# Kernel optimization log

Measured on AMD Instinct MI355X. Metric: run time of the kernel, lower is better.

## Reference

```python
import jax, jax.numpy as jnp
import numpy as np

OUT_DIM = 4096
NCROPS = 10
STUDENT_TEMP = 0.1
WARMUP_TEACHER_TEMP = 0.04
TEACHER_TEMP = 0.07
WARMUP_EPOCHS = 30
NEPOCHS = 100
B = 32
NG = 196
NL = 36
DFEAT = 384


def _l2norm(x, eps=1e-12):
    n = jnp.sqrt(jnp.sum(x * x, axis=-1, keepdims=True))
    return x / jnp.maximum(n, eps)


def setup_inputs() -> dict:
    key = jax.random.key(0)
    ks = jax.random.split(key, 6)
    s_rows = B * (2 * NG + (NCROPS - 2) * NL)  # 21760
    t_rows = 2 * B * NG  # 12544
    return {
        "student_cls_pred": jax.random.normal(ks[0], (NCROPS * B, OUT_DIM), jnp.float32),
        "student_region_pred": jax.random.normal(ks[1], (s_rows, OUT_DIM), jnp.float32),
        "student_feats": jax.random.normal(ks[2], (s_rows, DFEAT), jnp.float32),
        "teacher_cls_pred": jax.random.normal(ks[3], (2 * B, OUT_DIM), jnp.float32),
        "teacher_region_pred": jax.random.normal(ks[4], (t_rows, OUT_DIM), jnp.float32),
        "teacher_feats": jax.random.normal(ks[5], (t_rows, DFEAT), jnp.float32),
        "center": jnp.zeros((1, OUT_DIM), jnp.float32),
        "center_grid": jnp.zeros((1, OUT_DIM), jnp.float32),
        "epoch": 50,
        "n_global": 196,
        "n_local": 36,
    }


def reference(student_cls_pred, student_region_pred, student_feats,
              teacher_cls_pred, teacher_region_pred, teacher_feats,
              center, center_grid, epoch, n_global, n_local):
    sched = np.concatenate((np.linspace(WARMUP_TEACHER_TEMP, TEACHER_TEMP, WARMUP_EPOCHS),
                            np.ones(NEPOCHS - WARMUP_EPOCHS) * TEACHER_TEMP))
    temp = float(sched[epoch])

    b = teacher_cls_pred.shape[0] // 2
    N = n_global

    # teacher targets (detached in torch)
    t_cls = jax.lax.stop_gradient(jax.nn.softmax((teacher_cls_pred - center) / temp, axis=-1))
    t_reg = jax.lax.stop_gradient(jax.nn.softmax((teacher_region_pred - center_grid) / temp, axis=-1))
    t_cls_chunks = jnp.split(t_cls, 2, axis=0)
    t_reg_chunks = jnp.split(t_reg, 2, axis=0)
    t_fea_chunks = jnp.split(teacher_feats, 2, axis=0)

    s_cls = student_cls_pred / STUDENT_TEMP
    s_cls_chunks = jnp.split(s_cls, NCROPS, axis=0)

    split_sizes = [n_global] * 2 + [n_local] * (NCROPS - 2)
    offsets = np.cumsum([0] + [s * b for s in split_sizes])
    s_reg_scaled = student_region_pred / STUDENT_TEMP
    s_reg_chunks = [s_reg_scaled[offsets[k]:offsets[k + 1]] for k in range(NCROPS)]
    s_fea_chunks = [student_feats[offsets[k]:offsets[k + 1]] for k in range(NCROPS)]

    total_loss = jnp.zeros((), student_cls_pred.dtype)
    n_terms = 0
    for i in range(2):
        q = t_cls_chunks[i]                                   # [b, D]
        t_region = t_reg_chunks[i].reshape(b, N, -1)          # [b, N, D]
        t_fea = _l2norm(t_fea_chunks[i].reshape(b, N, -1))    # [b, N, F]
        for j in range(NCROPS):
            if j == i:
                continue
            v = s_cls_chunks[j]
            loss = 0.5 * jnp.sum(-q * jax.nn.log_softmax(v, axis=-1), axis=-1)  # [b]

            S = split_sizes[j]
            s_region = s_reg_chunks[j].reshape(b, S, -1)      # [b, S, D]
            s_fea = _l2norm(s_fea_chunks[j].reshape(b, S, -1))
            sim = jnp.einsum('bsf,bnf->bsn', s_fea, t_fea)    # cosine sim [b, S, N]
            ind = jnp.argmax(sim, axis=2)                     # [b, S]
            t_indexed = jnp.take_along_axis(t_region, ind[:, :, None], axis=1)  # [b, S, D]
            loss = loss + 0.5 * jnp.mean(
                jnp.sum(-t_indexed * jax.nn.log_softmax(s_region, axis=-1), axis=-1), axis=-1)
            total_loss = total_loss + jnp.mean(loss)
            n_terms += 1
    return total_loss / n_terms
```

## Files before the change

kernel.cpp:

```cpp
#include <hip/hip_runtime.h>
#include <math.h>

#define D 4096
#define F 384
#define NB 32
#define NG 196
#define NL 36
#define SROWS 21760
#define TROWS 12544
#define TCHUNK 6272
#define LCHUNK 1152
#define NPART (SROWS + 576)
#define KT 32
#define PADW 68

__device__ inline float get_invtemp(const int* ep_ptr) {
  int ep = *ep_ptr;
  double t = (ep < 30) ? (0.04 + (double)ep * (0.03 / 29.0)) : 0.07;
  return 1.0f / (float)t;
}

__device__ inline float warp_max(float v) {
#pragma unroll
  for (int o = 32; o; o >>= 1) v = fmaxf(v, __shfl_xor(v, o));
  return v;
}
__device__ inline float warp_sum(float v) {
#pragma unroll
  for (int o = 32; o; o >>= 1) v += __shfl_xor(v, o);
  return v;
}
__device__ inline float block_max(float v, float* sc) {
  v = warp_max(v);
  __syncthreads();
  if ((threadIdx.x & 63) == 0) sc[threadIdx.x >> 6] = v;
  __syncthreads();
  return fmaxf(fmaxf(sc[0], sc[1]), fmaxf(sc[2], sc[3]));
}
__device__ inline float block_sum(float v, float* sc) {
  v = warp_sum(v);
  __syncthreads();
  if ((threadIdx.x & 63) == 0) sc[threadIdx.x >> 6] = v;
  __syncthreads();
  return (sc[0] + sc[1]) + (sc[2] + sc[3]);
}

__device__ inline unsigned long long umax64(unsigned long long a, unsigned long long b) {
  return a > b ? a : b;
}
__device__ inline unsigned long long pack_key(float sim, int tc) {
  unsigned bts = __float_as_uint(sim);
  bts = (bts & 0x80000000u) ? ~bts : (bts | 0x80000000u);
  return ((unsigned long long)bts << 32) | (unsigned long long)(0xFFFFFFFFu - (unsigned)tc);
}
__device__ inline void unpack4(float4 v, float* dst) {
  dst[0] = v.x; dst[1] = v.y; dst[2] = v.z; dst[3] = v.w;
}

__device__ inline int srow_of(int cat, int b, int p) {
  if (cat == 0) return b * NG + p;
  if (cat == 1) return TCHUNK + b * NG + p;
  int j = p / 36;
  int pos = p - j * 36;
  return 2 * TCHUNK + j * LCHUNK + b * NL + pos;
}

__global__ __launch_bounds__(256) void k_tnorm(const float* __restrict__ tfea,
                                               float* __restrict__ invtn) {
  int gw = (blockIdx.x * 256 + threadIdx.x) >> 6;
  int lane = threadIdx.x & 63;
  if (gw >= TROWS) return;
  const float* p = tfea + (size_t)gw * F;
  float ss = 0.f;
#pragma unroll
  for (int k = 0; k < 6; k++) { float v = p[lane + 64 * k]; ss += v * v; }
  ss = warp_sum(ss);
  if (lane == 0) invtn[gw] = 1.0f / fmaxf(sqrtf(ss), 1e-12f);
}

__global__ __launch_bounds__(256) void k_sim(const float* __restrict__ sfea,
                                             const float* __restrict__ tfea,
                                             const float* __restrict__ invtn,
                                             unsigned long long* __restrict__ keys) {
  __shared__ float s_km[KT][PADW];
  __shared__ float tA_km[KT][PADW];
  __shared__ float tB_km[KT][PADW];
  int tid = threadIdx.x;
  int bid = blockIdx.x;
  int tt = bid & 3;
  int rest = bid >> 2;
  int st = rest % 13;
  int b = rest / 13;
  int cat, base_p;
  if (st < 4)      { cat = 0; base_p = st * 64; }
  else if (st < 8) { cat = 1; base_p = (st - 4) * 64; }
  else             { cat = 2; base_p = (st - 8) * 64; }
  int vs = ((cat < 2) ? NG : 288) - base_p; if (vs > 64) vs = 64;
  bool ni2 = (cat == 2);
  int iA = (cat == 0) ? 1 : 0;
  int tc0 = tt * 64;
  int vt = NG - tc0; if (vt > 64) vt = 64;
  int gA = iA * TCHUNK + b * NG + tc0;
  int gB = TCHUNK + b * NG + tc0;
  int tx = tid & 15, ty = tid >> 4;

  int row0 = tid >> 3, c4 = tid & 7;
  int row1 = row0 + 32;
  bool sv0 = row0 < vs, sv1 = row1 < vs;
  bool tv0 = row0 < vt, tv1 = row1 < vt;
  const float* sp0 = sfea + (size_t)srow_of(cat, b, base_p + (sv0 ? row0 : 0)) * F + c4 * 4;
  const float* sp1 = sfea + (size_t)srow_of(cat, b, base_p + (sv1 ? row1 : 0)) * F + c4 * 4;
  const float* tpA0 = tfea + (size_t)(gA + (tv0 ? row0 : 0)) * F + c4 * 4;
  const float* tpA1 = tfea + (size_t)(gA + (tv1 ? row1 : 0)) * F + c4 * 4;
  const float* tpB0 = tfea + (size_t)(gB + (tv0 ? row0 : 0)) * F + c4 * 4;
  const float* tpB1 = tfea + (size_t)(gB + (tv1 ? row1 : 0)) * F + c4 * 4;
  int kbase = c4 * 4;

  float accA[4][4] = {{0.f}}, accB[4][4] = {{0.f}};
  const float4 z4 = make_float4(0.f, 0.f, 0.f, 0.f);

  for (int kt = 0; kt < F / KT; kt++) {
    int k0 = kt * KT;
    float4 a0 = sv0 ? *(const float4*)(sp0 + k0) : z4;
    float4 a1 = sv1 ? *(const float4*)(sp1 + k0) : z4;
    float4 b0 = tv0 ? *(const float4*)(tpA0 + k0) : z4;
    float4 b1 = tv1 ? *(const float4*)(tpA1 + k0) : z4;
    float4 c0 = z4, c1 = z4;
    if (ni2) {
      c0 = tv0 ? *(const float4*)(tpB0 + k0) : z4;
      c1 = tv1 ? *(const float4*)(tpB1 + k0) : z4;
    }
    __syncthreads();
    s_km[kbase + 0][row0] = a0.x; s_km[kbase + 1][row0] = a0.y;
    s_km[kbase + 2][row0] = a0.z; s_km[kbase + 3][row0] = a0.w;
    s_km[kbase + 0][row1] = a1.x; s_km[kbase + 1][row1] = a1.y;
    s_km[kbase + 2][row1] = a1.z; s_km[kbase + 3][row1] = a1.w;
    tA_km[kbase + 0][row0] = b0.x; tA_km[kbase + 1][row0] = b0.y;
    tA_km[kbase + 2][row0] = b0.z; tA_km[kbase + 3][row0] = b0.w;
    tA_km[kbase + 0][row1] = b1.x; tA_km[kbase + 1][row1] = b1.y;
    tA_km[kbase + 2][row1] = b1.z; tA_km[kbase + 3][row1] = b1.w;
    if (ni2) {
      tB_km[kbase + 0][row0] = c0.x; tB_km[kbase + 1][row0] = c0.y;
      tB_km[kbase + 2][row0] = c0.z; tB_km[kbase + 3][row0] = c0.w;
      tB_km[kbase + 0][row1] = c1.x; tB_km[kbase + 1][row1] = c1.y;
      tB_km[kbase + 2][row1] = c1.z; tB_km[kbase + 3][row1] = c1.w;
    }
    __syncthreads();
    if (ni2) {
#pragma unroll 8
      for (int kk = 0; kk < KT; kk++) {
        float4 s4 = *(const float4*)&s_km[kk][ty * 4];
        float4 t4 = *(const float4*)&tA_km[kk][tx * 4];
        float4 u4 = *(const float4*)&tB_km[kk][tx * 4];
        float sv[4], tv[4], uv[4];
        unpack4(s4, sv); unpack4(t4, tv); unpack4(u4, uv);
#pragma unroll
        for (int m = 0; m < 4; m++)
#pragma unroll
          for (int n = 0; n < 4; n++) {
            accA[m][n] += sv[m] * tv[n];
            accB[m][n] += sv[m] * uv[n];
          }
      }
    } else {
#pragma unroll 8
      for (int kk = 0; kk < KT; kk++) {
        float4 s4 = *(const float4*)&s_km[kk][ty * 4];
        float4 t4 = *(const float4*)&tA_km[kk][tx * 4];
        float sv[4], tv[4];
        unpack4(s4, sv); unpack4(t4, tv);
#pragma unroll
        for (int m = 0; m < 4; m++)
#pragma unroll
          for (int n = 0; n < 4; n++) accA[m][n] += sv[m] * tv[n];
      }
    }
  }

  float invA[4], invB[4];
#pragma unroll
  for (int n = 0; n < 4; n++) {
    int tcl = tx * 4 + n;
    invA[n] = (tcl < vt) ? invtn[gA + tcl] : 0.f;
    invB[n] = (ni2 && tcl < vt) ? invtn[gB + tcl] : 0.f;
  }
#pragma unroll
  for (int m = 0; m < 4; m++) {
    int sl = ty * 4 + m;
    unsigned long long bestA = 0ull, bestB = 0ull;
#pragma unroll
    for (int n = 0; n < 4; n++) {
      int tcl = tx * 4 + n;
      if (tcl < vt) {
        int tc = tc0 + tcl;
        bestA = umax64(bestA, pack_key(accA[m][n] * invA[n], tc));
        if (ni2) bestB = umax64(bestB, pack_key(accB[m][n] * invB[n], tc));
      }
    }
#pragma unroll
    for (int o = 1; o < 16; o <<= 1) {
      bestA = umax64(bestA, __shfl_xor(bestA, o));
      bestB = umax64(bestB, __shfl_xor(bestB, o));
    }
    if (tx == 0 && sl < vs) {
      int sr = srow_of(cat, b, base_p + sl);
      atomicMax(&keys[(size_t)iA * SROWS + sr], bestA);
      if (ni2) atomicMax(&keys[(size_t)SROWS + sr], bestB);
    }
  }
}

__global__ __launch_bounds__(256) void k_region(const float* __restrict__ sreg,
                                                const float* __restrict__ treg,
                                                const float* __restrict__ cgrid,
                                                const unsigned long long* __restrict__ keys,
                                                const int* __restrict__ epoch,
                                                float* __restrict__ partials) {
  __shared__ float sc[4];
  int r = blockIdx.x, tid = threadIdx.x;
  int j, rem;
  if (r < TCHUNK)          { j = 0; rem = r; }
  else if (r < 2 * TCHUNK) { j = 1; rem = r - TCHUNK; }
  else { int q = r - 2 * TCHUNK; j = 2 + q / LCHUNK; rem = q - (j - 2) * LCHUNK; }
  int S = (j < 2) ? NG : NL;
  int b = rem / S;
  float invtemp = get_invtemp(epoch);

  const float4* sp = (const float4*)(sreg + (size_t)r * D);
  float sv[16];
  unpack4(sp[tid], sv); unpack4(sp[tid + 256], sv + 4);
  unpack4(sp[tid + 512], sv + 8); unpack4(sp[tid + 768], sv + 12);
#pragma unroll
  for (int k = 0; k < 16; k++) sv[k] *= 10.f;

  float m = -INFINITY;
#pragma unroll
  for (int k = 0; k < 16; k++) m = fmaxf(m, sv[k]);
  float M = block_max(m, sc);
  float e = 0.f;
#pragma unroll
  for (int k = 0; k < 16; k++) e += expf(sv[k] - M);
  float Ssum = block_sum(e, sc);
  float base = M + logf(Ssum);

  const float4* cp = (const float4*)cgrid;
  float cv[16];
  unpack4(cp[tid], cv); unpack4(cp[tid + 256], cv + 4);
  unpack4(cp[tid + 512], cv + 8); unpack4(cp[tid + 768], cv + 12);

  int ni = (j >= 2) ? 2 : 1;
  int i0 = (j == 0) ? 1 : 0;
  float wsel = 0.5f / (float)(S * NB * 18);
  float acc = 0.f;
  for (int q = 0; q < ni; q++) {
    int i = (q == 0) ? i0 : 1;
    unsigned long long kv = keys[(size_t)i * SROWS + r];
    int ind = (int)(0xFFFFFFFFu - (unsigned)(kv & 0xFFFFFFFFull));
    const float4* tp = (const float4*)(treg + (size_t)(i * TCHUNK + b * NG + ind) * D);
    float tv[16];
    unpack4(tp[tid], tv); unpack4(tp[tid + 256], tv + 4);
    unpack4(tp[tid + 512], tv + 8); unpack4(tp[tid + 768], tv + 12);
#pragma unroll
    for (int k = 0; k < 16; k++) tv[k] = (tv[k] - cv[k]) * invtemp;
    float tm = -INFINITY;
#pragma unroll
    for (int k = 0; k < 16; k++) tm = fmaxf(tm, tv[k]);
    float Tm = block_max(tm, sc);
    float es = 0.f, ed = 0.f;
#pragma unroll
    for (int k = 0; k < 16; k++) {
      float ee = expf(tv[k] - Tm);
      es += ee; ed += ee * sv[k];
    }
    es = block_sum(es, sc);
    ed = block_sum(ed, sc);
    acc += wsel * (base - ed / es);
  }
  if (tid == 0) partials[r] = acc;
}

__global__ __launch_bounds__(256) void k_cls(const float* __restrict__ scls,
                                             const float* __restrict__ tcls,
                                             const float* __restrict__ center,
                                             const int* __restrict__ epoch,
                                             float* __restrict__ part) {
  __shared__ float sc[4];
  int bid = blockIdx.x, tid = threadIdx.x;
  int p = bid >> 5, b = bid & 31;
  int i = p / 9, jj = p % 9;
  int j = (jj < i) ? jj : jj + 1;
  float invtemp = get_invtemp(epoch);

  const float4* sp = (const float4*)(scls + (size_t)(j * NB + b) * D);
  float sv[16];
  unpack4(sp[tid], sv); unpack4(sp[tid + 256], sv + 4);
  unpack4(sp[tid + 512], sv + 8); unpack4(sp[tid + 768], sv + 12);
#pragma unroll
  for (int k = 0; k < 16; k++) sv[k] *= 10.f;
  float m = -INFINITY;
#pragma unroll
  for (int k = 0; k < 16; k++) m = fmaxf(m, sv[k]);
  float M = block_max(m, sc);
  float e = 0.f;
#pragma unroll
  for (int k = 0; k < 16; k++) e += expf(sv[k] - M);
  float Ssum = block_sum(e, sc);
  float base = M + logf(Ssum);

  const float4* cp = (const float4*)center;
  const float4* tp = (const float4*)(tcls + (size_t)(i * NB + b) * D);
  float tv[16], cv[16];
  unpack4(cp[tid], cv); unpack4(cp[tid + 256], cv + 4);
  unpack4(cp[tid + 512], cv + 8); unpack4(cp[tid + 768], cv + 12);
  unpack4(tp[tid], tv); unpack4(tp[tid + 256], tv + 4);
  unpack4(tp[tid + 512], tv + 8); unpack4(tp[tid + 768], tv + 12);
#pragma unroll
  for (int k = 0; k < 16; k++) tv[k] = (tv[k] - cv[k]) * invtemp;
  float tm = -INFINITY;
#pragma unroll
  for (int k = 0; k < 16; k++) tm = fmaxf(tm, tv[k]);
  float Tm = block_max(tm, sc);
  float es = 0.f, ed = 0.f;
#pragma unroll
  for (int k = 0; k < 16; k++) {
    float ee = expf(tv[k] - Tm);
    es += ee; ed += ee * sv[k];
  }
  es = block_sum(es, sc);
  ed = block_sum(ed, sc);
  if (tid == 0) part[bid] = (base - ed / es) * (0.5f / 576.f);
}

__global__ __launch_bounds__(1024) void k_final(const float* __restrict__ partials,
                                                float* __restrict__ out, int n) {
  __shared__ float sc[16];
  int tid = threadIdx.x;
  float s = 0.f;
  for (int idx = tid; idx < n; idx += 1024) s += partials[idx];
  s = warp_sum(s);
  if ((tid & 63) == 0) sc[tid >> 6] = s;
  __syncthreads();
  if (tid < 64) {
    float v = (tid < 16) ? sc[tid] : 0.f;
    v = warp_sum(v);
    if (tid == 0) out[0] = v;
  }
}

extern "C" void kernel_launch(void* const* d_in, const int* in_sizes, int n_in,
                              void* d_out, int out_size, void* d_ws, size_t ws_size,
                              hipStream_t stream) {
  const float* s_cls = (const float*)d_in[0];
  const float* s_reg = (const float*)d_in[1];
  const float* s_fea = (const float*)d_in[2];
  const float* t_cls = (const float*)d_in[3];
  const float* t_reg = (const float*)d_in[4];
  const float* t_fea = (const float*)d_in[5];
  const float* center = (const float*)d_in[6];
  const float* cgrid = (const float*)d_in[7];
  const int* epoch = (const int*)d_in[8];

  char* ws = (char*)d_ws;
  unsigned long long* keys = (unsigned long long*)ws;
  float* invtn = (float*)(ws + 348160);
  float* partials = (float*)(ws + 398336);

  hipMemsetAsync(keys, 0, (size_t)2 * SROWS * sizeof(unsigned long long), stream);
  k_tnorm<<<TROWS / 4, 256, 0, stream>>>(t_fea, invtn);
  k_sim<<<32 * 13 * 4, 256, 0, stream>>>(s_fea, t_fea, invtn, keys);
  k_region<<<SROWS, 256, 0, stream>>>(s_reg, t_reg, cgrid, keys, epoch, partials);
  k_cls<<<576, 256, 0, stream>>>(s_cls, t_cls, center, epoch, partials + SROWS);
  k_final<<<1, 1024, 0, stream>>>(partials, (float*)d_out, NPART);
}
```

Before: 795.6 us.

## Precompute teacher softmax stats per row and rebalance similarity tiling

```diff
diff --git a/kernel.cpp b/kernel.cpp
--- a/kernel.cpp
+++ b/kernel.cpp
@@ -44,6 +44,18 @@
   __syncthreads();
   return (sc[0] + sc[1]) + (sc[2] + sc[3]);
 }
+__device__ inline void block_sum2(float a, float b, float* sc, float* ra, float* rb) {
+#pragma unroll
+  for (int o = 32; o; o >>= 1) { a += __shfl_xor(a, o); b += __shfl_xor(b, o); }
+  __syncthreads();
+  if ((threadIdx.x & 63) == 0) {
+    sc[threadIdx.x >> 6] = a;
+    sc[4 + (threadIdx.x >> 6)] = b;
+  }
+  __syncthreads();
+  *ra = (sc[0] + sc[1]) + (sc[2] + sc[3]);
+  *rb = (sc[4] + sc[5]) + (sc[6] + sc[7]);
+}
 
 __device__ inline unsigned long long umax64(unsigned long long a, unsigned long long b) {
   return a > b ? a : b;
@@ -76,6 +88,33 @@
   for (int k = 0; k < 6; k++) { float v = p[lane + 64 * k]; ss += v * v; }
   ss = warp_sum(ss);
   if (lane == 0) invtn[gw] = 1.0f / fmaxf(sqrtf(ss), 1e-12f);
+}
+
+__global__ __launch_bounds__(256) void k_tstat(const float* __restrict__ treg,
+                                               const float* __restrict__ cgrid,
+                                               const int* __restrict__ epoch,
+                                               float2* __restrict__ tstat) {
+  __shared__ float sc[8];
+  int r = blockIdx.x, tid = threadIdx.x;
+  float invt = get_invtemp(epoch);
+  const float4* tp = (const float4*)(treg + (size_t)r * D);
+  const float4* cp = (const float4*)cgrid;
+  float tv[16], cv[16];
+  unpack4(tp[tid], tv); unpack4(tp[tid + 256], tv + 4);
+  unpack4(tp[tid + 512], tv + 8); unpack4(tp[tid + 768], tv + 12);
+  unpack4(cp[tid], cv); unpack4(cp[tid + 256], cv + 4);
+  unpack4(cp[tid + 512], cv + 8); unpack4(cp[tid + 768], cv + 12);
+#pragma unroll
+  for (int k = 0; k < 16; k++) tv[k] = (tv[k] - cv[k]) * invt;
+  float m = -INFINITY;
+#pragma unroll
+  for (int k = 0; k < 16; k++) m = fmaxf(m, tv[k]);
+  float Tm = block_max(m, sc);
+  float e = 0.f;
+#pragma unroll
+  for (int k = 0; k < 16; k++) e += expf(tv[k] - Tm);
+  float es = block_sum(e, sc);
+  if (tid == 0) tstat[r] = make_float2(Tm, es);
 }
 
 __global__ __launch_bounds__(256) void k_sim(const float* __restrict__ sfea,
@@ -87,33 +126,41 @@
   __shared__ float tB_km[KT][PADW];
   int tid = threadIdx.x;
   int bid = blockIdx.x;
-  int tt = bid & 3;
-  int rest = bid >> 2;
-  int st = rest % 13;
-  int b = rest / 13;
-  int cat, base_p;
-  if (st < 4)      { cat = 0; base_p = st * 64; }
-  else if (st < 8) { cat = 1; base_p = (st - 4) * 64; }
-  else             { cat = 2; base_p = (st - 8) * 64; }
+  int w = bid % 36, b = bid / 36;
+  int cat, base_p, tcA0, tcB0, iA;
+  if (w < 16) {
+    cat = w >> 3;
+    int rest = w & 7;
+    base_p = (rest >> 1) * 64;
+    int tt = rest & 1;
+    tcA0 = tt * 128; tcB0 = tt * 128 + 64;
+    iA = (cat == 0) ? 1 : 0;
+  } else {
+    int w2 = w - 16;
+    cat = 2;
+    base_p = (w2 >> 2) * 64;
+    int tt = w2 & 3;
+    tcA0 = tt * 64; tcB0 = tt * 64;
+    iA = 0;
+  }
   int vs = ((cat < 2) ? NG : 288) - base_p; if (vs > 64) vs = 64;
-  bool ni2 = (cat == 2);
-  int iA = (cat == 0) ? 1 : 0;
-  int tc0 = tt * 64;
-  int vt = NG - tc0; if (vt > 64) vt = 64;
-  int gA = iA * TCHUNK + b * NG + tc0;
-  int gB = TCHUNK + b * NG + tc0;
+  int vtA = NG - tcA0; if (vtA > 64) vtA = 64;
+  int vtB = NG - tcB0; if (vtB > 64) vtB = 64;
+  int gA = iA * TCHUNK + b * NG + tcA0;
+  int gB = ((cat < 2) ? iA : 1) * TCHUNK + b * NG + tcB0;
   int tx = tid & 15, ty = tid >> 4;
 
   int row0 = tid >> 3, c4 = tid & 7;
   int row1 = row0 + 32;
   bool sv0 = row0 < vs, sv1 = row1 < vs;
-  bool tv0 = row0 < vt, tv1 = row1 < vt;
+  bool av0 = row0 < vtA, av1 = row1 < vtA;
+  bool bv0 = row0 < vtB, bv1 = row1 < vtB;
   const float* sp0 = sfea + (size_t)srow_of(cat, b, base_p + (sv0 ? row0 : 0)) * F + c4 * 4;
   const float* sp1 = sfea + (size_t)srow_of(cat, b, base_p + (sv1 ? row1 : 0)) * F + c4 * 4;
-  const float* tpA0 = tfea + (size_t)(gA + (tv0 ? row0 : 0)) * F + c4 * 4;
-  const float* tpA1 = tfea + (size_t)(gA + (tv1 ? row1 : 0)) * F + c4 * 4;
-  const float* tpB0 = tfea + (size_t)(gB + (tv0 ? row0 : 0)) * F + c4 * 4;
-  const float* tpB1 = tfea + (size_t)(gB + (tv1 ? row1 : 0)) * F + c4 * 4;
+  const float* tpA0 = tfea + (size_t)(gA + (av0 ? row0 : 0)) * F + c4 * 4;
+  const float* tpA1 = tfea + (size_t)(gA + (av1 ? row1 : 0)) * F + c4 * 4;
+  const float* tpB0 = tfea + (size_t)(gB + (bv0 ? row0 : 0)) * F + c4 * 4;
+  const float* tpB1 = tfea + (size_t)(gB + (bv1 ? row1 : 0)) * F + c4 * 4;
   int kbase = c4 * 4;
 
   float accA[4][4] = {{0.f}}, accB[4][4] = {{0.f}};
@@ -123,13 +170,10 @@
     int k0 = kt * KT;
     float4 a0 = sv0 ? *(const float4*)(sp0 + k0) : z4;
     float4 a1 = sv1 ? *(const float4*)(sp1 + k0) : z4;
-    float4 b0 = tv0 ? *(const float4*)(tpA0 + k0) : z4;
-    float4 b1 = tv1 ? *(const float4*)(tpA1 + k0) : z4;
-    float4 c0 = z4, c1 = z4;
-    if (ni2) {
-      c0 = tv0 ? *(const float4*)(tpB0 + k0) : z4;
-      c1 = tv1 ? *(const float4*)(tpB1 + k0) : z4;
-    }
+    float4 b0 = av0 ? *(const float4*)(tpA0 + k0) : z4;
+    float4 b1 = av1 ? *(const float4*)(tpA1 + k0) : z4;
+    float4 d0 = bv0 ? *(const float4*)(tpB0 + k0) : z4;
+    float4 d1 = bv1 ? *(const float4*)(tpB1 + k0) : z4;
     __syncthreads();
     s_km[kbase + 0][row0] = a0.x; s_km[kbase + 1][row0] = a0.y;
     s_km[kbase + 2][row0] = a0.z; s_km[kbase + 3][row0] = a0.w;
@@ -139,41 +183,25 @@
     tA_km[kbase + 2][row0] = b0.z; tA_km[kbase + 3][row0] = b0.w;
     tA_km[kbase + 0][row1] = b1.x; tA_km[kbase + 1][row1] = b1.y;
     tA_km[kbase + 2][row1] = b1.z; tA_km[kbase + 3][row1] = b1.w;
-    if (ni2) {
-      tB_km[kbase + 0][row0] = c0.x; tB_km[kbase + 1][row0] = c0.y;
-      tB_km[kbase + 2][row0] = c0.z; tB_km[kbase + 3][row0] = c0.w;
-      tB_km[kbase + 0][row1] = c1.x; tB_km[kbase + 1][row1] = c1.y;
-      tB_km[kbase + 2][row1] = c1.z; tB_km[kbase + 3][row1] = c1.w;
-    }
+    tB_km[kbase + 0][row0] = d0.x; tB_km[kbase + 1][row0] = d0.y;
+    tB_km[kbase + 2][row0] = d0.z; tB_km[kbase + 3][row0] = d0.w;
+    tB_km[kbase + 0][row1] = d1.x; tB_km[kbase + 1][row1] = d1.y;
+    tB_km[kbase + 2][row1] = d1.z; tB_km[kbase + 3][row1] = d1.w;
     __syncthreads();
-    if (ni2) {
 #pragma unroll 8
-      for (int kk = 0; kk < KT; kk++) {
-        float4 s4 = *(const float4*)&s_km[kk][ty * 4];
-        float4 t4 = *(const float4*)&tA_km[kk][tx * 4];
-        float4 u4 = *(const float4*)&tB_km[kk][tx * 4];
-        float sv[4], tv[4], uv[4];
-        unpack4(s4, sv); unpack4(t4, tv); unpack4(u4, uv);
-#pragma unroll
-        for (int m = 0; m < 4; m++)
-#pragma unroll
-          for (int n = 0; n < 4; n++) {
-            accA[m][n] += sv[m] * tv[n];
-            accB[m][n] += sv[m] * uv[n];
-          }
-      }
-    } else {
-#pragma unroll 8
-      for (int kk = 0; kk < KT; kk++) {
-        float4 s4 = *(const float4*)&s_km[kk][ty * 4];
-        float4 t4 = *(const float4*)&tA_km[kk][tx * 4];
-        float sv[4], tv[4];
-        unpack4(s4, sv); unpack4(t4, tv);
-#pragma unroll
-        for (int m = 0; m < 4; m++)
-#pragma unroll
-          for (int n = 0; n < 4; n++) accA[m][n] += sv[m] * tv[n];
-      }
+    for (int kk = 0; kk < KT; kk++) {
+      float4 s4 = *(const float4*)&s_km[kk][ty * 4];
+      float4 t4 = *(const float4*)&tA_km[kk][tx * 4];
+      float4 u4 = *(const float4*)&tB_km[kk][tx * 4];
+      float sv[4], tv[4], uv[4];
+      unpack4(s4, sv); unpack4(t4, tv); unpack4(u4, uv);
+#pragma unroll
+      for (int m = 0; m < 4; m++)
+#pragma unroll
+        for (int n = 0; n < 4; n++) {
+          accA[m][n] += sv[m] * tv[n];
+          accB[m][n] += sv[m] * uv[n];
+        }
     }
   }
 
@@ -181,8 +209,8 @@
 #pragma unroll
   for (int n = 0; n < 4; n++) {
     int tcl = tx * 4 + n;
-    invA[n] = (tcl < vt) ? invtn[gA + tcl] : 0.f;
-    invB[n] = (ni2 && tcl < vt) ? invtn[gB + tcl] : 0.f;
+    invA[n] = (tcl < vtA) ? invtn[gA + tcl] : 0.f;
+    invB[n] = (tcl < vtB) ? invtn[gB + tcl] : 0.f;
   }
 #pragma unroll
   for (int m = 0; m < 4; m++) {
@@ -191,11 +219,8 @@
 #pragma unroll
     for (int n = 0; n < 4; n++) {
       int tcl = tx * 4 + n;
-      if (tcl < vt) {
-        int tc = tc0 + tcl;
-        bestA = umax64(bestA, pack_key(accA[m][n] * invA[n], tc));
-        if (ni2) bestB = umax64(bestB, pack_key(accB[m][n] * invB[n], tc));
-      }
+      if (tcl < vtA) bestA = umax64(bestA, pack_key(accA[m][n] * invA[n], tcA0 + tcl));
+      if (tcl < vtB) bestB = umax64(bestB, pack_key(accB[m][n] * invB[n], tcB0 + tcl));
     }
 #pragma unroll
     for (int o = 1; o < 16; o <<= 1) {
@@ -204,8 +229,12 @@
     }
     if (tx == 0 && sl < vs) {
       int sr = srow_of(cat, b, base_p + sl);
-      atomicMax(&keys[(size_t)iA * SROWS + sr], bestA);
-      if (ni2) atomicMax(&keys[(size_t)SROWS + sr], bestB);
+      if (cat < 2) {
+        atomicMax(&keys[(size_t)iA * SROWS + sr], umax64(bestA, bestB));
+      } else {
+        atomicMax(&keys[sr], bestA);
+        atomicMax(&keys[(size_t)SROWS + sr], bestB);
+      }
     }
   }
 }
@@ -214,9 +243,10 @@
                                                 const float* __restrict__ treg,
                                                 const float* __restrict__ cgrid,
                                                 const unsigned long long* __restrict__ keys,
+                                                const float2* __restrict__ tstat,
                                                 const int* __restrict__ epoch,
                                                 float* __restrict__ partials) {
-  __shared__ float sc[4];
+  __shared__ float sc[8];
   int r = blockIdx.x, tid = threadIdx.x;
   int j, rem;
   if (r < TCHUNK)          { j = 0; rem = r; }
@@ -224,7 +254,7 @@
   else { int q = r - 2 * TCHUNK; j = 2 + q / LCHUNK; rem = q - (j - 2) * LCHUNK; }
   int S = (j < 2) ? NG : NL;
   int b = rem / S;
-  float invtemp = get_invtemp(epoch);
+  float invt = get_invtemp(epoch);
 
   const float4* sp = (const float4*)(sreg + (size_t)r * D);
   float sv[16];
@@ -248,33 +278,49 @@
   unpack4(cp[tid], cv); unpack4(cp[tid + 256], cv + 4);
   unpack4(cp[tid + 512], cv + 8); unpack4(cp[tid + 768], cv + 12);
 
-  int ni = (j >= 2) ? 2 : 1;
-  int i0 = (j == 0) ? 1 : 0;
   float wsel = 0.5f / (float)(S * NB * 18);
-  float acc = 0.f;
-  for (int q = 0; q < ni; q++) {
-    int i = (q == 0) ? i0 : 1;
-    unsigned long long kv = keys[(size_t)i * SROWS + r];
+  float acc;
+  if (j < 2) {
+    int i0 = (j == 0) ? 1 : 0;
+    unsigned long long kv = keys[(size_t)i0 * SROWS + r];
     int ind = (int)(0xFFFFFFFFu - (unsigned)(kv & 0xFFFFFFFFull));
-    const float4* tp = (const float4*)(treg + (size_t)(i * TCHUNK + b * NG + ind) * D);
+    int trow = i0 * TCHUNK + b * NG + ind;
+    float2 st = tstat[trow];
+    const float4* tp = (const float4*)(treg + (size_t)trow * D);
     float tv[16];
     unpack4(tp[tid], tv); unpack4(tp[tid + 256], tv + 4);
     unpack4(tp[tid + 512], tv + 8); unpack4(tp[tid + 768], tv + 12);
-#pragma unroll
-    for (int k = 0; k < 16; k++) tv[k] = (tv[k] - cv[k]) * invtemp;
-    float tm = -INFINITY;
-#pragma unroll
-    for (int k = 0; k < 16; k++) tm = fmaxf(tm, tv[k]);
-    float Tm = block_max(tm, sc);
-    float es = 0.f, ed = 0.f;
+    float d = 0.f;
+#pragma unroll
+    for (int k = 0; k < 16; k++)
+      d += expf((tv[k] - cv[k]) * invt - st.x) * sv[k];
+    float ed = block_sum(d, sc);
+    acc = wsel * (base - ed / st.y);
+  } else {
+    unsigned long long kv0 = keys[r];
+    unsigned long long kv1 = keys[(size_t)SROWS + r];
+    int ind0 = (int)(0xFFFFFFFFu - (unsigned)(kv0 & 0xFFFFFFFFull));
+    int ind1 = (int)(0xFFFFFFFFu - (unsigned)(kv1 & 0xFFFFFFFFull));
+    int trow0 = b * NG + ind0;
+    int trow1 = TCHUNK + b * NG + ind1;
+    float2 st0 = tstat[trow0];
+    float2 st1 = tstat[trow1];
+    const float4* tp0 = (const float4*)(treg + (size_t)trow0 * D);
+    const float4* tp1 = (const float4*)(treg + (size_t)trow1 * D);
+    float tv0[16], tv1[16];
+    unpack4(tp0[tid], tv0); unpack4(tp1[tid], tv1);
+    unpack4(tp0[tid + 256], tv0 + 4); unpack4(tp1[tid + 256], tv1 + 4);
+    unpack4(tp0[tid + 512], tv0 + 8); unpack4(tp1[tid + 512], tv1 + 8);
+    unpack4(tp0[tid + 768], tv0 + 12); unpack4(tp1[tid + 768], tv1 + 12);
+    float d0 = 0.f, d1 = 0.f;
 #pragma unroll
     for (int k = 0; k < 16; k++) {
-      float ee = expf(tv[k] - Tm);
-      es += ee; ed += ee * sv[k];
+      d0 += expf((tv0[k] - cv[k]) * invt - st0.x) * sv[k];
+      d1 += expf((tv1[k] - cv[k]) * invt - st1.x) * sv[k];
     }
-    es = block_sum(es, sc);
-    ed = block_sum(ed, sc);
-    acc += wsel * (base - ed / es);
+    float ed0, ed1;
+    block_sum2(d0, d1, sc, &ed0, &ed1);
+    acc = wsel * ((base - ed0 / st0.y) + (base - ed1 / st1.y));
   }
   if (tid == 0) partials[r] = acc;
 }
@@ -284,7 +330,7 @@
                                              const float* __restrict__ center,
                                              const int* __restrict__ epoch,
                                              float* __restrict__ part) {
-  __shared__ float sc[4];
+  __shared__ float sc[8];
   int bid = blockIdx.x, tid = threadIdx.x;
   int p = bid >> 5, b = bid & 31;
   int i = p / 9, jj = p % 9;
@@ -363,12 +409,14 @@
   char* ws = (char*)d_ws;
   unsigned long long* keys = (unsigned long long*)ws;
   float* invtn = (float*)(ws + 348160);
-  float* partials = (float*)(ws + 398336);
+  float2* tstat = (float2*)(ws + 398336);
+  float* partials = (float*)(ws + 498688);
 
   hipMemsetAsync(keys, 0, (size_t)2 * SROWS * sizeof(unsigned long long), stream);
   k_tnorm<<<TROWS / 4, 256, 0, stream>>>(t_fea, invtn);
-  k_sim<<<32 * 13 * 4, 256, 0, stream>>>(s_fea, t_fea, invtn, keys);
-  k_region<<<SROWS, 256, 0, stream>>>(s_reg, t_reg, cgrid, keys, epoch, partials);
+  k_tstat<<<TROWS, 256, 0, stream>>>(t_reg, cgrid, epoch, tstat);
+  k_sim<<<32 * 36, 256, 0, stream>>>(s_fea, t_fea, invtn, keys);
+  k_region<<<SROWS, 256, 0, stream>>>(s_reg, t_reg, cgrid, keys, tstat, epoch, partials);
   k_cls<<<576, 256, 0, stream>>>(s_cls, t_cls, center, epoch, partials + SROWS);
   k_final<<<1, 1024, 0, stream>>>(partials, (float*)d_out, NPART);
 }
```

Result: no change. 796.1 us (+0.1%).
